# Kernel tuning notes

Measured on AMD Instinct MI355X. Metric: run time of the kernel, lower is better.

The kernel has to match this reference:

```python
import jax, jax.numpy as jnp
import numpy as np

B, T, D, H, L, K = 64, 512, 256, 256, 2, 3


def setup_inputs() -> dict:
    key = jax.random.key(0)
    ks = jax.random.split(key, 12)
    s = 0.05
    f = jnp.float32
    return {
        "x": jax.random.normal(ks[0], (B, T, D), f),
        # GRUCell params per layer (torch gate order: r, z, n)
        "W_ih": jax.random.normal(ks[1], (L, 3 * H, H), f) * s,
        "b_ih": jax.random.normal(ks[2], (L, 3 * H), f) * s,
        "W_hh": jax.random.normal(ks[3], (L, 3 * H, H), f) * s,
        "b_hh": jax.random.normal(ks[4], (L, 3 * H), f) * s,
        # refinement cell params per layer
        "Wg": jax.random.normal(ks[5], (L, H, 2 * H), f) * s,
        "bg": jax.random.normal(ks[6], (L, H), f) * s,
        "Wt": jax.random.normal(ks[7], (L, H, 2 * H), f) * s,
        "bt": jax.random.normal(ks[8], (L, H), f) * s,
        "Wu": jax.random.normal(ks[9], (L, H, H), f) * s,
        "bu": jax.random.normal(ks[10], (L, H), f) * s,
    }


def reference(x, W_ih, b_ih, W_hh, b_hh, Wg, bg, Wt, bt, Wu, bu):
    def step(hidden, x_t):  # hidden: (L, B, H), x_t: (B, D)
        inp = x_t
        new_hiddens = []
        for l in range(L):
            h = hidden[l]
            # GRU cell (torch semantics)
            gi = inp @ W_ih[l].T + b_ih[l]
            gh = h @ W_hh[l].T + b_hh[l]
            i_r, i_z, i_n = jnp.split(gi, 3, axis=-1)
            h_r, h_z, h_n = jnp.split(gh, 3, axis=-1)
            r = jax.nn.sigmoid(i_r + h_r)
            z = jax.nn.sigmoid(i_z + h_z)
            n = jnp.tanh(i_n + r * h_n)
            h_new = (1.0 - z) * n + z * h
            # recursive refinement
            out = h_new
            rh = h_new
            for _ in range(K):
                comb = jnp.concatenate([out, rh], axis=-1)  # (B, 2H)
                g = jax.nn.sigmoid(comb @ Wg[l].T + bg[l])
                ref = jnp.tanh(comb @ Wt[l].T + bt[l])
                out = g * ref + (1.0 - g) * out
                rh = jnp.tanh(out @ Wu[l].T + bu[l])
            new_hiddens.append(h_new)
            inp = out
        return jnp.stack(new_hiddens, axis=0), inp

    hidden0 = jnp.zeros((L, B, H), x.dtype)
    final_hidden, outs = jax.lax.scan(step, hidden0, jnp.swapaxes(x, 0, 1))
    output = jnp.swapaxes(outs, 0, 1)  # (B, T, H)
    return output, final_hidden
```

## Files before the change

kernel.cpp:

```cpp
#include <hip/hip_runtime.h>

typedef float  f32x4  __attribute__((ext_vector_type(4)));
typedef __bf16 bf16x8 __attribute__((ext_vector_type(8)));

#define NB 64
#define NT 512
#define ND 256
#define NH 256
#define NROW (NB*NT)

#define OFF_WIH 0
#define OFF_WHH 393216
#define OFF_WGT 786432
#define OFF_WU  1310720
#define W_TOTAL 1441792
#define OFF_GI   (W_TOTAL)
#define OFF_OUT0 (OFF_GI + 512*64*768)
#define OFF_OUT1 (OFF_OUT0 + NROW*256)
#define OFF_FLAG (OFF_OUT1 + NROW*256)

#define NW 192

__device__ inline unsigned short f2bu(float f){
  unsigned int u = __builtin_bit_cast(unsigned int, f);
  unsigned int r = u + 0x7fffu + ((u >> 16) & 1u);
  return (unsigned short)(r >> 16);
}
__device__ inline float bf2f(unsigned short u){
  unsigned int v = ((unsigned int)u) << 16;
  return __builtin_bit_cast(float, v);
}
__device__ inline float sigm(float x){ return 1.0f / (1.0f + __expf(-x)); }
__device__ inline float tanhf_(float x){ return 1.0f - 2.0f / (__expf(2.0f * x) + 1.0f); }

#define MFMA(a,b,c) __builtin_amdgcn_mfma_f32_16x16x32_bf16((a),(b),(c),0,0,0)

__device__ inline void gload_lds16(const void* g, void* l){
  __builtin_amdgcn_global_load_lds(
    (const __attribute__((address_space(1))) unsigned int*)g,
    (__attribute__((address_space(3))) unsigned int*)l, 16, 0, 0);
}
__device__ inline bf16x8 ldG(const unsigned short* p){
  return *reinterpret_cast<const bf16x8*>(p);
}
template<int SLP>
__device__ inline void spin_ge(int* p, int tgt){
  while (__hip_atomic_load(p, __ATOMIC_RELAXED, __HIP_MEMORY_SCOPE_AGENT) < tgt)
    __builtin_amdgcn_s_sleep(SLP);
}

__global__ void cvt_weights(const float* __restrict__ Wih, const float* __restrict__ Whh,
                            const float* __restrict__ Wg,  const float* __restrict__ Wt,
                            const float* __restrict__ Wu,  unsigned short* __restrict__ ws){
  int i = blockIdx.x * blockDim.x + threadIdx.x;
  if (i < OFF_WHH) {
    ws[i] = f2bu(Wih[i]);
  } else if (i < OFF_WGT) {
    ws[i] = f2bu(Whh[i - OFF_WHH]);
  } else if (i < OFF_WU) {
    int j = i - OFF_WGT;
    int l = j >> 18; int r = (j >> 9) & 511; int k = j & 511;
    float v = (r < 256) ? Wg[(l * 256 + r) * 512 + k]
                        : Wt[(l * 256 + (r - 256)) * 512 + k];
    ws[i] = f2bu(v);
  } else if (i < W_TOTAL) {
    ws[i] = f2bu(Wu[i - OFF_WU]);
  }
}

__global__ void pack_x(const float* __restrict__ x, unsigned short* __restrict__ xin){
  size_t i = ((size_t)blockIdx.x * blockDim.x + threadIdx.x) * 4;
  float4 v = *reinterpret_cast<const float4*>(x + i);
  ushort4 u; u.x = f2bu(v.x); u.y = f2bu(v.y); u.z = f2bu(v.z); u.w = f2bu(v.w);
  *reinterpret_cast<ushort4*>(xin + i) = u;
}

__global__ __launch_bounds__(1024) void gi_gemm(
    const unsigned short* __restrict__ xin,
    const unsigned short* __restrict__ wih,
    const float* __restrict__ bih, const float* __restrict__ bhh,
    unsigned short* __restrict__ gi)
{
  __shared__ alignas(16) unsigned short sA[64 * 256];
  const int tid = threadIdx.x, blk = blockIdx.x;
  const int ln = tid & 63, wv = tid >> 6, m = ln & 15, lg = ln >> 4;
  {
    const char* src = (const char*)(xin + (size_t)blk * 64 * 256);
    #pragma unroll
    for (int i = 0; i < 2; ++i){
      int o = tid * 16 + i * 16384;
      int r = o >> 9, wb = o & 511;
      gload_lds16(src + (size_t)r * 512 + (wb ^ ((r & 7) << 4)), (char*)sA + o);
    }
  }
  __syncthreads();
  f32x4 acc[3][4] = {};
  #pragma unroll
  for (int kc = 0; kc < 8; ++kc){
    int kk = kc * 32 + lg * 8;
    bf16x8 a[4];
    #pragma unroll
    for (int mt = 0; mt < 4; ++mt){
      int row = mt * 16 + m;
      a[mt] = *(const bf16x8*)((const char*)sA + row * 512 + ((kk * 2) ^ ((row & 7) << 4)));
    }
    #pragma unroll
    for (int g = 0; g < 3; ++g){
      bf16x8 b = ldG(wih + (size_t)(g * 256 + wv * 16 + m) * 256 + kk);
      #pragma unroll
      for (int mt = 0; mt < 4; ++mt) acc[g][mt] = MFMA(a[mt], b, acc[g][mt]);
    }
  }
  const int c = wv * 16 + m;
  #pragma unroll
  for (int g = 0; g < 3; ++g){
    float bias = bih[g * 256 + c] + (g < 2 ? bhh[g * 256 + c] : 0.f);
    #pragma unroll
    for (int mt = 0; mt < 4; ++mt){
      #pragma unroll
      for (int j = 0; j < 4; ++j){
        int row = blk * 64 + mt * 16 + lg * 4 + j;
        int b = row >> 9, t = row & 511;
        gi[((size_t)t * 64 + b) * 768 + g * 256 + c] = f2bu(acc[g][mt][j] + bias);
      }
    }
  }
}

__device__ void chain_role(
    int grp, const unsigned short* __restrict__ gi, const unsigned short* __restrict__ whh,
    const float* __restrict__ bhh, unsigned short* __restrict__ outw,
    float* __restrict__ hfin, int* prog, int* bd, char* smem)
{
  __builtin_amdgcn_s_setprio(1);
  char* hAc = smem;
  const int tid = threadIdx.x;
  const int ln  = tid & 63, wv = tid >> 6;
  const int m   = ln & 15;
  const int lg  = ln >> 4;

  f32x4 wf[3][2][8];
  #pragma unroll
  for (int g = 0; g < 3; ++g)
    #pragma unroll
    for (int s = 0; s < 2; ++s){
      const unsigned short* p = whh + (size_t)(g * 256 + wv * 32 + s * 16 + m) * 256;
      #pragma unroll
      for (int kc = 0; kc < 8; ++kc){
        wf[g][s][kc] = *reinterpret_cast<const f32x4*>(p + kc * 32 + lg * 8);
        asm volatile("" : "+v"(wf[g][s][kc]));
      }
    }

  const int bb   = lg & 1;
  const int su   = lg >> 1;
  const int wcol = wv * 32 + su * 16 + m;
  const int brow = grp * 2 + bb;
  const float bNv = bhh[512 + wcol];

  const int arow  = m & 1;
  const int arows = arow << 4;
  const int rbase = arow * 512;
  const int wbyte = bb * 512 + ((wcol * 2) ^ (bb << 4));

  const unsigned short* gbase = gi + (size_t)brow * 768 + wcol;
  unsigned short* op = outw + (size_t)brow * NT * 256 + wcol;

  if (tid < 256){
    ((unsigned int*)hAc)[tid] = 0;
    ((unsigned int*)(hAc + 1024))[tid] = 0;
  }
  if (bd){
    if (tid == 0){ spin_ge<8>(&bd[0], 16); spin_ge<8>(&bd[1], 16); __threadfence(); }
    __syncthreads();
    (void)__hip_atomic_load(&bd[0], __ATOMIC_ACQUIRE, __HIP_MEMORY_SCOPE_AGENT);
  }
  unsigned int gAr = gbase[0], gAz = gbase[256], gAn = gbase[512];
  unsigned int gBr = gbase[49152], gBz = gbase[49152 + 256], gBn = gbase[49152 + 512];
  float h = 0.f;
  __syncthreads();

  auto body = [&](int t, int curo, unsigned int& GR, unsigned int& GZ, unsigned int& GN){
    float xr = bf2f((unsigned short)GR);
    float xz = bf2f((unsigned short)GZ);
    float xn = bf2f((unsigned short)GN);
    if (t + 2 < NT){
      const unsigned short* gp = gbase + (size_t)(t + 2) * 49152;
      GR = gp[0]; GZ = gp[256]; GN = gp[512];
    }
    f32x4 a00{}, a01{}, a10{}, a11{}, a20{}, a21{};
    #pragma unroll
    for (int kc = 0; kc < 8; ++kc){
      int kb = kc * 64 + lg * 16;
      bf16x8 hv = *(const bf16x8*)(hAc + curo + rbase + (kb ^ arows));
      a00 = MFMA(hv, __builtin_bit_cast(bf16x8, wf[0][0][kc]), a00);
      a01 = MFMA(hv, __builtin_bit_cast(bf16x8, wf[0][1][kc]), a01);
      a10 = MFMA(hv, __builtin_bit_cast(bf16x8, wf[1][0][kc]), a10);
      a11 = MFMA(hv, __builtin_bit_cast(bf16x8, wf[1][1][kc]), a11);
      a20 = MFMA(hv, __builtin_bit_cast(bf16x8, wf[2][0][kc]), a20);
      a21 = MFMA(hv, __builtin_bit_cast(bf16x8, wf[2][1][kc]), a21);
    }
    float aR = su ? (bb ? a01[1] : a01[0]) : (bb ? a00[1] : a00[0]);
    float aZ = su ? (bb ? a11[1] : a11[0]) : (bb ? a10[1] : a10[0]);
    float aN = su ? (bb ? a21[1] : a21[0]) : (bb ? a20[1] : a20[0]);
    float R = sigm(aR + xr);
    float Z = sigm(aZ + xz);
    float N = tanhf_(xn + R * (aN + bNv));
    h = N + Z * (h - N);
    unsigned short hb = f2bu(h);
    *(unsigned short*)(hAc + (curo ^ 1024) + wbyte) = hb;
    op[t * 256] = hb;
    asm volatile("s_waitcnt lgkmcnt(0)" ::: "memory");
    __builtin_amdgcn_sched_barrier(0);
    __builtin_amdgcn_s_barrier();
    __builtin_amdgcn_sched_barrier(0);
  };

  for (int tp = 0; tp < NT; tp += 2){
    if ((tp & 15) == 0){
      if (tp > 0){
        __syncthreads();
        if (tid == 0){
          __threadfence();
          __hip_atomic_store(prog, tp, __ATOMIC_RELEASE, __HIP_MEMORY_SCOPE_AGENT);
        }
      }
      if (bd){
        int B1 = (tp >> 4) + 1;
        if (B1 < 32){
          if (tid == 0){ spin_ge<8>(&bd[B1], 16); __threadfence(); }
          __syncthreads();
          (void)__hip_atomic_load(&bd[B1], __ATOMIC_ACQUIRE, __HIP_MEMORY_SCOPE_AGENT);
        }
      }
    }
    body(tp,     0,    gAr, gAz, gAn);
    body(tp + 1, 1024, gBr, gBz, gBn);
  }
  __syncthreads();
  if (tid == 0){
    __threadfence();
    __hip_atomic_store(prog, NT, __ATOMIC_RELEASE, __HIP_MEMORY_SCOPE_AGENT);
  }
  hfin[(size_t)brow * 256 + wcol] = h;
}

__device__ void worker_role(
    int w, unsigned short* __restrict__ gi,
    const unsigned short* __restrict__ outw0, const unsigned short* __restrict__ outw1,
    const unsigned short* __restrict__ wsb,
    const float* __restrict__ bih, const float* __restrict__ bhh,
    const float* __restrict__ bg, const float* __restrict__ bt, const float* __restrict__ bu,
    float* __restrict__ o, int* flags, char* smem)
{
  const int tid = threadIdx.x;
  const int ln = tid & 63, wv = tid >> 6, m = ln & 15, lg = ln >> 4;

  auto ldA = [&](int row, int kbyte) -> bf16x8 {
    return *(const bf16x8*)(smem + row * 1024 + (kbyte ^ ((row & 7) << 4)));
  };

  for (int i = w; i < 1024; i += NW){
    const int lay = i >> 9, t = i & 511;
    int* prog = &flags[lay * 32];
    if (tid == 0){
      for (int q = 0; q < 32; ++q) spin_ge<32>(&prog[q], t + 1);
      __threadfence();
    }
    __syncthreads();
    (void)__hip_atomic_load(&prog[0], __ATOMIC_ACQUIRE, __HIP_MEMORY_SCOPE_AGENT);

    const unsigned short* src0 = lay ? outw1 : outw0;
    #pragma unroll
    for (int q = 0; q < 8; ++q){
      int ofs = tid * 16 + q * 8192;
      int r = ofs >> 10, wb = ofs & 1023;
      int wb2 = (wb ^ ((r & 7) << 4)) & 511;
      gload_lds16((const char*)(src0 + ((size_t)r * NT + t) * 256) + wb2, smem + ofs);
    }
    __syncthreads();

    const unsigned short* wgt = wsb + OFF_WGT + (size_t)lay * 512 * 512;
    const unsigned short* wu  = wsb + OFF_WU  + (size_t)lay * 256 * 256;
    const float* bgp = bg + lay * 256;
    const float* btp = bt + lay * 256;
    const float* bup = bu + lay * 256;

    for (int iter = 0; iter < 3; ++iter){
      float oo0[4][4], oo1[4][4];
      {
        f32x4 ag0[4] = {}, at0[4] = {}, ag1[4] = {}, at1[4] = {};
        #pragma unroll 2
        for (int kc = 0; kc < 16; ++kc){
          int kk = kc * 32 + lg * 8;
          bf16x8 A[4];
          #pragma unroll
          for (int mt = 0; mt < 4; ++mt) A[mt] = ldA(mt * 16 + m, kk * 2);
          bf16x8 Bg0 = ldG(wgt + (size_t)(      wv * 32 + m) * 512 + kk);
          bf16x8 Bt0 = ldG(wgt + (size_t)(256 + wv * 32 + m) * 512 + kk);
          bf16x8 Bg1 = ldG(wgt + (size_t)(      wv * 32 + 16 + m) * 512 + kk);
          bf16x8 Bt1 = ldG(wgt + (size_t)(256 + wv * 32 + 16 + m) * 512 + kk);
          #pragma unroll
          for (int mt = 0; mt < 4; ++mt){
            ag0[mt] = MFMA(A[mt], Bg0, ag0[mt]);
            at0[mt] = MFMA(A[mt], Bt0, at0[mt]);
            ag1[mt] = MFMA(A[mt], Bg1, ag1[mt]);
            at1[mt] = MFMA(A[mt], Bt1, at1[mt]);
          }
        }
        int c0 = wv * 32 + m, c1 = wv * 32 + 16 + m;
        float bg0 = bgp[c0], bt0 = btp[c0], bg1 = bgp[c1], bt1 = btp[c1];
        #pragma unroll
        for (int mt = 0; mt < 4; ++mt)
          #pragma unroll
          for (int j = 0; j < 4; ++j){
            int row = mt * 16 + lg * 4 + j;
            float old0 = bf2f(*(unsigned short*)(smem + row * 1024 + ((c0 * 2) ^ ((row & 7) << 4))));
            float old1 = bf2f(*(unsigned short*)(smem + row * 1024 + ((c1 * 2) ^ ((row & 7) << 4))));
            float g0 = sigm(ag0[mt][j] + bg0);
            float r0 = tanhf_(at0[mt][j] + bt0);
            float g1 = sigm(ag1[mt][j] + bg1);
            float r1 = tanhf_(at1[mt][j] + bt1);
            oo0[mt][j] = g0 * r0 + (1.f - g0) * old0;
            oo1[mt][j] = g1 * r1 + (1.f - g1) * old1;
          }
      }
      __syncthreads();
      if (iter == 2 && lay == 1){
        #pragma unroll
        for (int mt = 0; mt < 4; ++mt)
          #pragma unroll
          for (int j = 0; j < 4; ++j){
            int b = mt * 16 + lg * 4 + j;
            o[((size_t)b * NT + t) * 256 + wv * 32 + m]      = oo0[mt][j];
            o[((size_t)b * NT + t) * 256 + wv * 32 + 16 + m] = oo1[mt][j];
          }
      } else {
        #pragma unroll
        for (int mt = 0; mt < 4; ++mt)
          #pragma unroll
          for (int j = 0; j < 4; ++j){
            int row = mt * 16 + lg * 4 + j;
            int c0 = wv * 32 + m, c1 = wv * 32 + 16 + m;
            *(unsigned short*)(smem + row * 1024 + ((c0 * 2) ^ ((row & 7) << 4))) = f2bu(oo0[mt][j]);
            *(unsigned short*)(smem + row * 1024 + ((c1 * 2) ^ ((row & 7) << 4))) = f2bu(oo1[mt][j]);
          }
        __syncthreads();
        if (iter < 2){
          f32x4 au0[4] = {}, au1[4] = {};
          #pragma unroll 2
          for (int kc = 0; kc < 8; ++kc){
            int kk = kc * 32 + lg * 8;
            bf16x8 A[4];
            #pragma unroll
            for (int mt = 0; mt < 4; ++mt) A[mt] = ldA(mt * 16 + m, kk * 2);
            bf16x8 Bu0 = ldG(wu + (size_t)(wv * 32 + m) * 256 + kk);
            bf16x8 Bu1 = ldG(wu + (size_t)(wv * 32 + 16 + m) * 256 + kk);
            #pragma unroll
            for (int mt = 0; mt < 4; ++mt){
              au0[mt] = MFMA(A[mt], Bu0, au0[mt]);
              au1[mt] = MFMA(A[mt], Bu1, au1[mt]);
            }
          }
          int c0 = wv * 32 + m, c1 = wv * 32 + 16 + m;
          float bu0 = bup[c0], bu1 = bup[c1];
          #pragma unroll
          for (int mt = 0; mt < 4; ++mt)
            #pragma unroll
            for (int j = 0; j < 4; ++j){
              int row = mt * 16 + lg * 4 + j;
              *(unsigned short*)(smem + row * 1024 + (((512 + c0 * 2)) ^ ((row & 7) << 4)))
                  = f2bu(tanhf_(au0[mt][j] + bu0));
              *(unsigned short*)(smem + row * 1024 + (((512 + c1 * 2)) ^ ((row & 7) << 4)))
                  = f2bu(tanhf_(au1[mt][j] + bu1));
            }
          __syncthreads();
        }
      }
    }
    if (lay == 0){
      const unsigned short* wih1 = wsb + OFF_WIH + (size_t)768 * 256;
      #pragma unroll
      for (int qp = 0; qp < 3; ++qp){
        int cg0 = (wv + 8 * (2 * qp)) * 16 + m;
        int cg1 = (wv + 8 * (2 * qp + 1)) * 16 + m;
        f32x4 acc0[4] = {}, acc1[4] = {};
        #pragma unroll
        for (int kc = 0; kc < 8; ++kc){
          int kk = kc * 32 + lg * 8;
          bf16x8 A[4];
          #pragma unroll
          for (int mt = 0; mt < 4; ++mt) A[mt] = ldA(mt * 16 + m, kk * 2);
          bf16x8 B0 = ldG(wih1 + (size_t)cg0 * 256 + kk);
          bf16x8 B1 = ldG(wih1 + (size_t)cg1 * 256 + kk);
          #pragma unroll
          for (int mt = 0; mt < 4; ++mt){
            acc0[mt] = MFMA(A[mt], B0, acc0[mt]);
            acc1[mt] = MFMA(A[mt], B1, acc1[mt]);
          }
        }
        float b0 = bih[768 + cg0] + (cg0 < 512 ? bhh[768 + cg0] : 0.f);
        float b1 = bih[768 + cg1] + (cg1 < 512 ? bhh[768 + cg1] : 0.f);
        #pragma unroll
        for (int mt = 0; mt < 4; ++mt)
          #pragma unroll
          for (int j = 0; j < 4; ++j){
            int b = mt * 16 + lg * 4 + j;
            gi[((size_t)t * 64 + b) * 768 + cg0] = f2bu(acc0[mt][j] + b0);
            gi[((size_t)t * 64 + b) * 768 + cg1] = f2bu(acc1[mt][j] + b1);
          }
      }
      __syncthreads();
      if (tid == 0){
        __threadfence();
        __hip_atomic_fetch_add(&flags[64 + (t >> 4)], 1, __ATOMIC_RELEASE, __HIP_MEMORY_SCOPE_AGENT);
      }
    } else {
      __syncthreads();
    }
  }
}

__global__ __launch_bounds__(512, 2) void mega(
    unsigned short* __restrict__ gi, const unsigned short* __restrict__ wsb,
    const float* __restrict__ bih, const float* __restrict__ bhh,
    const float* __restrict__ bg, const float* __restrict__ bt, const float* __restrict__ bu,
    unsigned short* __restrict__ outw0, unsigned short* __restrict__ outw1,
    float* __restrict__ o, float* __restrict__ hf, int* flags)
{
  __shared__ char smem[65536];
  const int role = blockIdx.x;
  if (role < NW){
    worker_role(role, gi, outw0, outw1, wsb, bih, bhh, bg, bt, bu, o, flags, smem);
  } else if (role < NW + 32){
    chain_role(role - NW, gi, wsb + OFF_WHH, bhh, outw0, hf,
               &flags[role - NW], nullptr, smem);
  } else {
    chain_role(role - NW - 32, gi, wsb + OFF_WHH + 768 * 256, bhh + 768, outw1,
               hf + 64 * 256, &flags[32 + (role - NW - 32)], &flags[64], smem);
  }
}

extern "C" void kernel_launch(void* const* d_in, const int* in_sizes, int n_in,
                              void* d_out, int out_size, void* d_ws, size_t ws_size,
                              hipStream_t stream) {
  const float* x   = (const float*)d_in[0];
  const float* Wih = (const float*)d_in[1];
  const float* bih = (const float*)d_in[2];
  const float* Whh = (const float*)d_in[3];
  const float* bhh = (const float*)d_in[4];
  const float* Wg  = (const float*)d_in[5];
  const float* bg  = (const float*)d_in[6];
  const float* Wt  = (const float*)d_in[7];
  const float* bt  = (const float*)d_in[8];
  const float* Wu  = (const float*)d_in[9];
  const float* bu  = (const float*)d_in[10];
  unsigned short* ws = (unsigned short*)d_ws;
  float* o  = (float*)d_out;
  float* hf = o + (size_t)NB * NT * NH;

  unsigned short* gi    = ws + OFF_GI;
  unsigned short* outw0 = ws + OFF_OUT0;
  unsigned short* outw1 = ws + OFF_OUT1;
  unsigned short* xin   = ws + OFF_OUT1;
  int* flags = (int*)(ws + OFF_FLAG);

  cvt_weights<<<W_TOTAL / 256, 256, 0, stream>>>(Wih, Whh, Wg, Wt, Wu, ws);
  pack_x<<<(NROW * 256 / 4) / 256, 256, 0, stream>>>(x, xin);
  gi_gemm<<<512, 1024, 0, stream>>>(xin, ws + OFF_WIH, bih, bhh, gi);
  (void)hipMemsetAsync(flags, 0, 96 * sizeof(int), stream);
  mega<<<NW + 64, 512, 0, stream>>>(gi, ws, bih, bhh, bg, bt, bu, outw0, outw1, o, hf, flags);
}
```

Measured before the change: 979.3 us.

## Dynamically schedule layer-1 refinement across all blocks and pad flags to cachelines

Worker blocks now handle only layer-0 refinement tasks with a static stride. Layer-1 refinement tasks are handed out through a global atomic counter that every block, including the chain blocks once they finish, pulls from. The progress and readiness flags are spread 32 ints apart so that each flag sits on its own cache line and spinning blocks do not falsely share lines. This is meant to cut tail latency and spin contention, at the cost of an extra atomic per task and a more complex dependency protocol.

```diff
diff --git a/kernel.cpp b/kernel.cpp
--- a/kernel.cpp
+++ b/kernel.cpp
@@ -18,6 +18,7 @@
 #define OFF_OUT0 (OFF_GI + 512*64*768)
 #define OFF_OUT1 (OFF_OUT0 + NROW*256)
 #define OFF_FLAG (OFF_OUT1 + NROW*256)
+#define FLAG_INTS 3073
 
 #define NW 192
 
@@ -171,7 +172,7 @@
     ((unsigned int*)(hAc + 1024))[tid] = 0;
   }
   if (bd){
-    if (tid == 0){ spin_ge<8>(&bd[0], 16); spin_ge<8>(&bd[1], 16); __threadfence(); }
+    if (tid == 0){ spin_ge<8>(&bd[0], 16); spin_ge<8>(&bd[32], 16); __threadfence(); }
     __syncthreads();
     (void)__hip_atomic_load(&bd[0], __ATOMIC_ACQUIRE, __HIP_MEMORY_SCOPE_AGENT);
   }
@@ -228,9 +229,9 @@
       if (bd){
         int B1 = (tp >> 4) + 1;
         if (B1 < 32){
-          if (tid == 0){ spin_ge<8>(&bd[B1], 16); __threadfence(); }
+          if (tid == 0){ spin_ge<8>(&bd[B1 * 32], 16); __threadfence(); }
           __syncthreads();
-          (void)__hip_atomic_load(&bd[B1], __ATOMIC_ACQUIRE, __HIP_MEMORY_SCOPE_AGENT);
+          (void)__hip_atomic_load(&bd[B1 * 32], __ATOMIC_ACQUIRE, __HIP_MEMORY_SCOPE_AGENT);
         }
       }
     }
@@ -243,11 +244,13 @@
     __hip_atomic_store(prog, NT, __ATOMIC_RELEASE, __HIP_MEMORY_SCOPE_AGENT);
   }
   hfin[(size_t)brow * 256 + wcol] = h;
-}
-
-__device__ void worker_role(
-    int w, unsigned short* __restrict__ gi,
-    const unsigned short* __restrict__ outw0, const unsigned short* __restrict__ outw1,
+  __builtin_amdgcn_s_setprio(0);
+  __syncthreads();
+}
+
+template<int LAY>
+__device__ void refine_task(
+    int t, unsigned short* __restrict__ gi, const unsigned short* __restrict__ src0,
     const unsigned short* __restrict__ wsb,
     const float* __restrict__ bih, const float* __restrict__ bhh,
     const float* __restrict__ bg, const float* __restrict__ bt, const float* __restrict__ bu,
@@ -260,164 +263,153 @@
     return *(const bf16x8*)(smem + row * 1024 + (kbyte ^ ((row & 7) << 4)));
   };
 
-  for (int i = w; i < 1024; i += NW){
-    const int lay = i >> 9, t = i & 511;
-    int* prog = &flags[lay * 32];
-    if (tid == 0){
-      for (int q = 0; q < 32; ++q) spin_ge<32>(&prog[q], t + 1);
-      __threadfence();
-    }
-    __syncthreads();
-    (void)__hip_atomic_load(&prog[0], __ATOMIC_ACQUIRE, __HIP_MEMORY_SCOPE_AGENT);
-
-    const unsigned short* src0 = lay ? outw1 : outw0;
-    #pragma unroll
-    for (int q = 0; q < 8; ++q){
-      int ofs = tid * 16 + q * 8192;
-      int r = ofs >> 10, wb = ofs & 1023;
-      int wb2 = (wb ^ ((r & 7) << 4)) & 511;
-      gload_lds16((const char*)(src0 + ((size_t)r * NT + t) * 256) + wb2, smem + ofs);
-    }
-    __syncthreads();
-
-    const unsigned short* wgt = wsb + OFF_WGT + (size_t)lay * 512 * 512;
-    const unsigned short* wu  = wsb + OFF_WU  + (size_t)lay * 256 * 256;
-    const float* bgp = bg + lay * 256;
-    const float* btp = bt + lay * 256;
-    const float* bup = bu + lay * 256;
-
-    for (int iter = 0; iter < 3; ++iter){
-      float oo0[4][4], oo1[4][4];
-      {
-        f32x4 ag0[4] = {}, at0[4] = {}, ag1[4] = {}, at1[4] = {};
+  #pragma unroll
+  for (int q = 0; q < 8; ++q){
+    int ofs = tid * 16 + q * 8192;
+    int r = ofs >> 10, wb = ofs & 1023;
+    int wb2 = (wb ^ ((r & 7) << 4)) & 511;
+    gload_lds16((const char*)(src0 + ((size_t)r * NT + t) * 256) + wb2, smem + ofs);
+  }
+  __syncthreads();
+
+  const unsigned short* wgt = wsb + OFF_WGT + (size_t)LAY * 512 * 512;
+  const unsigned short* wu  = wsb + OFF_WU  + (size_t)LAY * 256 * 256;
+  const float* bgp = bg + LAY * 256;
+  const float* btp = bt + LAY * 256;
+  const float* bup = bu + LAY * 256;
+
+  for (int iter = 0; iter < 3; ++iter){
+    float oo0[4][4], oo1[4][4];
+    {
+      f32x4 ag0[4] = {}, at0[4] = {}, ag1[4] = {}, at1[4] = {};
+      #pragma unroll 2
+      for (int kc = 0; kc < 16; ++kc){
+        int kk = kc * 32 + lg * 8;
+        bf16x8 A[4];
+        #pragma unroll
+        for (int mt = 0; mt < 4; ++mt) A[mt] = ldA(mt * 16 + m, kk * 2);
+        bf16x8 Bg0 = ldG(wgt + (size_t)(      wv * 32 + m) * 512 + kk);
+        bf16x8 Bt0 = ldG(wgt + (size_t)(256 + wv * 32 + m) * 512 + kk);
+        bf16x8 Bg1 = ldG(wgt + (size_t)(      wv * 32 + 16 + m) * 512 + kk);
+        bf16x8 Bt1 = ldG(wgt + (size_t)(256 + wv * 32 + 16 + m) * 512 + kk);
+        #pragma unroll
+        for (int mt = 0; mt < 4; ++mt){
+          ag0[mt] = MFMA(A[mt], Bg0, ag0[mt]);
+          at0[mt] = MFMA(A[mt], Bt0, at0[mt]);
+          ag1[mt] = MFMA(A[mt], Bg1, ag1[mt]);
+          at1[mt] = MFMA(A[mt], Bt1, at1[mt]);
+        }
+      }
+      int c0 = wv * 32 + m, c1 = wv * 32 + 16 + m;
+      float bg0 = bgp[c0], bt0 = btp[c0], bg1 = bgp[c1], bt1 = btp[c1];
+      #pragma unroll
+      for (int mt = 0; mt < 4; ++mt)
+        #pragma unroll
+        for (int j = 0; j < 4; ++j){
+          int row = mt * 16 + lg * 4 + j;
+          float old0 = bf2f(*(unsigned short*)(smem + row * 1024 + ((c0 * 2) ^ ((row & 7) << 4))));
+          float old1 = bf2f(*(unsigned short*)(smem + row * 1024 + ((c1 * 2) ^ ((row & 7) << 4))));
+          float g0 = sigm(ag0[mt][j] + bg0);
+          float r0 = tanhf_(at0[mt][j] + bt0);
+          float g1 = sigm(ag1[mt][j] + bg1);
+          float r1 = tanhf_(at1[mt][j] + bt1);
+          oo0[mt][j] = g0 * r0 + (1.f - g0) * old0;
+          oo1[mt][j] = g1 * r1 + (1.f - g1) * old1;
+        }
+    }
+    __syncthreads();
+    if (iter == 2 && LAY == 1){
+      #pragma unroll
+      for (int mt = 0; mt < 4; ++mt)
+        #pragma unroll
+        for (int j = 0; j < 4; ++j){
+          int b = mt * 16 + lg * 4 + j;
+          o[((size_t)b * NT + t) * 256 + wv * 32 + m]      = oo0[mt][j];
+          o[((size_t)b * NT + t) * 256 + wv * 32 + 16 + m] = oo1[mt][j];
+        }
+    } else {
+      #pragma unroll
+      for (int mt = 0; mt < 4; ++mt)
+        #pragma unroll
+        for (int j = 0; j < 4; ++j){
+          int row = mt * 16 + lg * 4 + j;
+          int c0 = wv * 32 + m, c1 = wv * 32 + 16 + m;
+          *(unsigned short*)(smem + row * 1024 + ((c0 * 2) ^ ((row & 7) << 4))) = f2bu(oo0[mt][j]);
+          *(unsigned short*)(smem + row * 1024 + ((c1 * 2) ^ ((row & 7) << 4))) = f2bu(oo1[mt][j]);
+        }
+      __syncthreads();
+      if (iter < 2){
+        f32x4 au0[4] = {}, au1[4] = {};
         #pragma unroll 2
-        for (int kc = 0; kc < 16; ++kc){
-          int kk = kc * 32 + lg * 8;
-          bf16x8 A[4];
-          #pragma unroll
-          for (int mt = 0; mt < 4; ++mt) A[mt] = ldA(mt * 16 + m, kk * 2);
-          bf16x8 Bg0 = ldG(wgt + (size_t)(      wv * 32 + m) * 512 + kk);
-          bf16x8 Bt0 = ldG(wgt + (size_t)(256 + wv * 32 + m) * 512 + kk);
-          bf16x8 Bg1 = ldG(wgt + (size_t)(      wv * 32 + 16 + m) * 512 + kk);
-          bf16x8 Bt1 = ldG(wgt + (size_t)(256 + wv * 32 + 16 + m) * 512 + kk);
-          #pragma unroll
-          for (int mt = 0; mt < 4; ++mt){
-            ag0[mt] = MFMA(A[mt], Bg0, ag0[mt]);
-            at0[mt] = MFMA(A[mt], Bt0, at0[mt]);
-            ag1[mt] = MFMA(A[mt], Bg1, ag1[mt]);
-            at1[mt] = MFMA(A[mt], Bt1, at1[mt]);
-          }
-        }
-        int c0 = wv * 32 + m, c1 = wv * 32 + 16 + m;
-        float bg0 = bgp[c0], bt0 = btp[c0], bg1 = bgp[c1], bt1 = btp[c1];
-        #pragma unroll
-        for (int mt = 0; mt < 4; ++mt)
-          #pragma unroll
-          for (int j = 0; j < 4; ++j){
-            int row = mt * 16 + lg * 4 + j;
-            float old0 = bf2f(*(unsigned short*)(smem + row * 1024 + ((c0 * 2) ^ ((row & 7) << 4))));
-            float old1 = bf2f(*(unsigned short*)(smem + row * 1024 + ((c1 * 2) ^ ((row & 7) << 4))));
-            float g0 = sigm(ag0[mt][j] + bg0);
-            float r0 = tanhf_(at0[mt][j] + bt0);
-            float g1 = sigm(ag1[mt][j] + bg1);
-            float r1 = tanhf_(at1[mt][j] + bt1);
-            oo0[mt][j] = g0 * r0 + (1.f - g0) * old0;
-            oo1[mt][j] = g1 * r1 + (1.f - g1) * old1;
-          }
-      }
-      __syncthreads();
-      if (iter == 2 && lay == 1){
-        #pragma unroll
-        for (int mt = 0; mt < 4; ++mt)
-          #pragma unroll
-          for (int j = 0; j < 4; ++j){
-            int b = mt * 16 + lg * 4 + j;
-            o[((size_t)b * NT + t) * 256 + wv * 32 + m]      = oo0[mt][j];
-            o[((size_t)b * NT + t) * 256 + wv * 32 + 16 + m] = oo1[mt][j];
-          }
-      } else {
-        #pragma unroll
-        for (int mt = 0; mt < 4; ++mt)
-          #pragma unroll
-          for (int j = 0; j < 4; ++j){
-            int row = mt * 16 + lg * 4 + j;
-            int c0 = wv * 32 + m, c1 = wv * 32 + 16 + m;
-            *(unsigned short*)(smem + row * 1024 + ((c0 * 2) ^ ((row & 7) << 4))) = f2bu(oo0[mt][j]);
-            *(unsigned short*)(smem + row * 1024 + ((c1 * 2) ^ ((row & 7) << 4))) = f2bu(oo1[mt][j]);
-          }
-        __syncthreads();
-        if (iter < 2){
-          f32x4 au0[4] = {}, au1[4] = {};
-          #pragma unroll 2
-          for (int kc = 0; kc < 8; ++kc){
-            int kk = kc * 32 + lg * 8;
-            bf16x8 A[4];
-            #pragma unroll
-            for (int mt = 0; mt < 4; ++mt) A[mt] = ldA(mt * 16 + m, kk * 2);
-            bf16x8 Bu0 = ldG(wu + (size_t)(wv * 32 + m) * 256 + kk);
-            bf16x8 Bu1 = ldG(wu + (size_t)(wv * 32 + 16 + m) * 256 + kk);
-            #pragma unroll
-            for (int mt = 0; mt < 4; ++mt){
-              au0[mt] = MFMA(A[mt], Bu0, au0[mt]);
-              au1[mt] = MFMA(A[mt], Bu1, au1[mt]);
-            }
-          }
-          int c0 = wv * 32 + m, c1 = wv * 32 + 16 + m;
-          float bu0 = bup[c0], bu1 = bup[c1];
-          #pragma unroll
-          for (int mt = 0; mt < 4; ++mt)
-            #pragma unroll
-            for (int j = 0; j < 4; ++j){
-              int row = mt * 16 + lg * 4 + j;
-              *(unsigned short*)(smem + row * 1024 + (((512 + c0 * 2)) ^ ((row & 7) << 4)))
-                  = f2bu(tanhf_(au0[mt][j] + bu0));
-              *(unsigned short*)(smem + row * 1024 + (((512 + c1 * 2)) ^ ((row & 7) << 4)))
-                  = f2bu(tanhf_(au1[mt][j] + bu1));
-            }
-          __syncthreads();
-        }
-      }
-    }
-    if (lay == 0){
-      const unsigned short* wih1 = wsb + OFF_WIH + (size_t)768 * 256;
-      #pragma unroll
-      for (int qp = 0; qp < 3; ++qp){
-        int cg0 = (wv + 8 * (2 * qp)) * 16 + m;
-        int cg1 = (wv + 8 * (2 * qp + 1)) * 16 + m;
-        f32x4 acc0[4] = {}, acc1[4] = {};
-        #pragma unroll
         for (int kc = 0; kc < 8; ++kc){
           int kk = kc * 32 + lg * 8;
           bf16x8 A[4];
           #pragma unroll
           for (int mt = 0; mt < 4; ++mt) A[mt] = ldA(mt * 16 + m, kk * 2);
-          bf16x8 B0 = ldG(wih1 + (size_t)cg0 * 256 + kk);
-          bf16x8 B1 = ldG(wih1 + (size_t)cg1 * 256 + kk);
+          bf16x8 Bu0 = ldG(wu + (size_t)(wv * 32 + m) * 256 + kk);
+          bf16x8 Bu1 = ldG(wu + (size_t)(wv * 32 + 16 + m) * 256 + kk);
           #pragma unroll
           for (int mt = 0; mt < 4; ++mt){
-            acc0[mt] = MFMA(A[mt], B0, acc0[mt]);
-            acc1[mt] = MFMA(A[mt], B1, acc1[mt]);
+            au0[mt] = MFMA(A[mt], Bu0, au0[mt]);
+            au1[mt] = MFMA(A[mt], Bu1, au1[mt]);
           }
         }
-        float b0 = bih[768 + cg0] + (cg0 < 512 ? bhh[768 + cg0] : 0.f);
-        float b1 = bih[768 + cg1] + (cg1 < 512 ? bhh[768 + cg1] : 0.f);
+        int c0 = wv * 32 + m, c1 = wv * 32 + 16 + m;
+        float bu0 = bup[c0], bu1 = bup[c1];
         #pragma unroll
         for (int mt = 0; mt < 4; ++mt)
           #pragma unroll
           for (int j = 0; j < 4; ++j){
-            int b = mt * 16 + lg * 4 + j;
-            gi[((size_t)t * 64 + b) * 768 + cg0] = f2bu(acc0[mt][j] + b0);
-            gi[((size_t)t * 64 + b) * 768 + cg1] = f2bu(acc1[mt][j] + b1);
+            int row = mt * 16 + lg * 4 + j;
+            *(unsigned short*)(smem + row * 1024 + (((512 + c0 * 2)) ^ ((row & 7) << 4)))
+                = f2bu(tanhf_(au0[mt][j] + bu0));
+            *(unsigned short*)(smem + row * 1024 + (((512 + c1 * 2)) ^ ((row & 7) << 4)))
+                = f2bu(tanhf_(au1[mt][j] + bu1));
           }
-      }
-      __syncthreads();
-      if (tid == 0){
-        __threadfence();
-        __hip_atomic_fetch_add(&flags[64 + (t >> 4)], 1, __ATOMIC_RELEASE, __HIP_MEMORY_SCOPE_AGENT);
-      }
-    } else {
-      __syncthreads();
-    }
+        __syncthreads();
+      }
+    }
+  }
+  if (LAY == 0){
+    const unsigned short* wih1 = wsb + OFF_WIH + (size_t)768 * 256;
+    #pragma unroll
+    for (int qp = 0; qp < 3; ++qp){
+      int cg0 = (wv + 8 * (2 * qp)) * 16 + m;
+      int cg1 = (wv + 8 * (2 * qp + 1)) * 16 + m;
+      f32x4 acc0[4] = {}, acc1[4] = {};
+      #pragma unroll
+      for (int kc = 0; kc < 8; ++kc){
+        int kk = kc * 32 + lg * 8;
+        bf16x8 A[4];
+        #pragma unroll
+        for (int mt = 0; mt < 4; ++mt) A[mt] = ldA(mt * 16 + m, kk * 2);
+        bf16x8 B0 = ldG(wih1 + (size_t)cg0 * 256 + kk);
+        bf16x8 B1 = ldG(wih1 + (size_t)cg1 * 256 + kk);
+        #pragma unroll
+        for (int mt = 0; mt < 4; ++mt){
+          acc0[mt] = MFMA(A[mt], B0, acc0[mt]);
+          acc1[mt] = MFMA(A[mt], B1, acc1[mt]);
+        }
+      }
+      float b0 = bih[768 + cg0] + (cg0 < 512 ? bhh[768 + cg0] : 0.f);
+      float b1 = bih[768 + cg1] + (cg1 < 512 ? bhh[768 + cg1] : 0.f);
+      #pragma unroll
+      for (int mt = 0; mt < 4; ++mt)
+        #pragma unroll
+        for (int j = 0; j < 4; ++j){
+          int b = mt * 16 + lg * 4 + j;
+          gi[((size_t)t * 64 + b) * 768 + cg0] = f2bu(acc0[mt][j] + b0);
+          gi[((size_t)t * 64 + b) * 768 + cg1] = f2bu(acc1[mt][j] + b1);
+        }
+    }
+    __syncthreads();
+    if (tid == 0){
+      __threadfence();
+      __hip_atomic_fetch_add(&flags[2048 + (t >> 4) * 32], 1,
+                             __ATOMIC_RELEASE, __HIP_MEMORY_SCOPE_AGENT);
+    }
+  } else {
+    __syncthreads();
   }
 }
 
@@ -429,15 +421,42 @@
     float* __restrict__ o, float* __restrict__ hf, int* flags)
 {
   __shared__ char smem[65536];
+  __shared__ int jslot;
   const int role = blockIdx.x;
+  const int tid = threadIdx.x;
+
   if (role < NW){
-    worker_role(role, gi, outw0, outw1, wsb, bih, bhh, bg, bt, bu, o, flags, smem);
+    for (int t = role; t < 512; t += NW){
+      if (tid == 0){
+        for (int q = 0; q < 32; ++q) spin_ge<32>(&flags[q * 32], t + 1);
+        __threadfence();
+      }
+      __syncthreads();
+      (void)__hip_atomic_load(&flags[0], __ATOMIC_ACQUIRE, __HIP_MEMORY_SCOPE_AGENT);
+      refine_task<0>(t, gi, outw0, wsb, bih, bhh, bg, bt, bu, o, flags, smem);
+    }
   } else if (role < NW + 32){
     chain_role(role - NW, gi, wsb + OFF_WHH, bhh, outw0, hf,
-               &flags[role - NW], nullptr, smem);
+               &flags[(role - NW) * 32], nullptr, smem);
   } else {
     chain_role(role - NW - 32, gi, wsb + OFF_WHH + 768 * 256, bhh + 768, outw1,
-               hf + 64 * 256, &flags[32 + (role - NW - 32)], &flags[64], smem);
+               hf + 64 * 256, &flags[1024 + (role - NW - 32) * 32], &flags[2048], smem);
+  }
+
+  for (;;){
+    if (tid == 0)
+      jslot = __hip_atomic_fetch_add(&flags[3072], 1, __ATOMIC_RELAXED, __HIP_MEMORY_SCOPE_AGENT);
+    __syncthreads();
+    int t = jslot;
+    __syncthreads();
+    if (t >= 512) break;
+    if (tid == 0){
+      for (int q = 0; q < 32; ++q) spin_ge<32>(&flags[1024 + q * 32], t + 1);
+      __threadfence();
+    }
+    __syncthreads();
+    (void)__hip_atomic_load(&flags[1024], __ATOMIC_ACQUIRE, __HIP_MEMORY_SCOPE_AGENT);
+    refine_task<1>(t, gi, outw1, wsb, bih, bhh, bg, bt, bu, o, flags, smem);
   }
 }
 
@@ -468,6 +487,6 @@
   cvt_weights<<<W_TOTAL / 256, 256, 0, stream>>>(Wih, Whh, Wg, Wt, Wu, ws);
   pack_x<<<(NROW * 256 / 4) / 256, 256, 0, stream>>>(x, xin);
   gi_gemm<<<512, 1024, 0, stream>>>(xin, ws + OFF_WIH, bih, bhh, gi);
-  (void)hipMemsetAsync(flags, 0, 96 * sizeof(int), stream);
+  (void)hipMemsetAsync(flags, 0, FLAG_INTS * sizeof(int), stream);
   mega<<<NW + 64, 512, 0, stream>>>(gi, ws, bih, bhh, bg, bt, bu, outw0, outw1, o, hf, flags);
 }
```

Measured after the change: 1.092 ms. +11.5%, slower.
